# Performance work log

Hardware: AMD Instinct MI355X
Metric: run time of the kernel (lower is better)

## Reference

```python
import jax, jax.numpy as jnp
import numpy as np


def quat_to_rot(q):
    # q: [B, 4] = (x, y, z, w); same math as from_quaternion in the source.
    x, y, z, w = q[:, 0], q[:, 1], q[:, 2], q[:, 3]
    tx, ty, tz = 2.0 * x, 2.0 * y, 2.0 * z
    twx, twy, twz = tx * w, ty * w, tz * w
    txx, txy, txz = tx * x, ty * x, tz * x
    tyy, tyz, tzz = ty * y, tz * y, tz * z
    r = jnp.stack([1.0 - (tyy + tzz), txy - twz, txz + twy,
                   txy + twz, 1.0 - (txx + tzz), tyz - twx,
                   txz - twy, tyz + twx, 1.0 - (txx + tyy)], axis=-1)
    return r.reshape(-1, 3, 3)


def matrix_from_params(transfos):
    B, N = transfos.shape
    R = quat_to_rot(transfos[:, :4])
    if N == 10:
        S = jax.vmap(jnp.diag)(transfos[:, -3:])
    else:
        S = jnp.broadcast_to(jnp.eye(3, dtype=transfos.dtype), (B, 3, 3))
    SR = jnp.matmul(S, R)
    if N == 7:
        t = transfos[:, 4:7][..., None]
    else:
        t = jnp.zeros((B, 3, 1), transfos.dtype)
    return jnp.concatenate([SR, t], axis=2)  # [B, 3, 4]


def spatial_transformer_3d(img, transfos, min_ref_grid, max_ref_grid):
    B, H, W, D, C = img.shape  # ref_size_xyz = (W, H, D) per the source
    theta = matrix_from_params(transfos)  # [B, 3, 4]

    xs = jnp.linspace(min_ref_grid[0], max_ref_grid[0], W)
    ys = jnp.linspace(min_ref_grid[1], max_ref_grid[1], H)
    zs = jnp.linspace(min_ref_grid[2], max_ref_grid[2], D)
    mz, my, mx = jnp.meshgrid(zs, ys, xs, indexing='ij')  # (D, H, W), x fastest
    Nel = D * H * W
    grid = jnp.stack([mx.ravel(), my.ravel(), mz.ravel(),
                      jnp.ones(Nel, dtype=img.dtype)], axis=0)  # (4, Nel)
    pts = jnp.einsum('bij,jn->bin', theta, grid)  # (B, 3, Nel)

    Wf, Hf, Df = float(W), float(H), float(D)
    cx = (Wf - 1.0) / (max_ref_grid[0] - min_ref_grid[0])
    cy = (Hf - 1.0) / (max_ref_grid[1] - min_ref_grid[1])
    cz = (Df - 1.0) / (max_ref_grid[2] - min_ref_grid[2])
    ix = cx * pts[:, 0, :] - cx * min_ref_grid[0]
    iy = cy * pts[:, 1, :] - cy * min_ref_grid[1]
    iz = cz * pts[:, 2, :] - cz * min_ref_grid[2]

    # padding_mode in {'zeros','min'}: validity mask for out-of-grid points
    valid = ((ix >= 0.0) & (ix <= Wf - 1.0) &
             (iy >= 0.0) & (iy <= Hf - 1.0) &
             (iz >= 0.0) & (iz <= Df - 1.0)).astype(img.dtype)[..., None]  # (B, Nel, 1)

    ix0 = jnp.clip(jnp.floor(ix), 0.0, Wf - 1.0)
    iy0 = jnp.clip(jnp.floor(iy), 0.0, Hf - 1.0)
    iz0 = jnp.clip(jnp.floor(iz), 0.0, Df - 1.0)

    imf = img.reshape(B, H * W * D, C)
    acc = jnp.zeros((B, Nel, C), img.dtype)
    for ox in (0.0, 1.0):
        for oy in (0.0, 1.0):
            for oz in (0.0, 1.0):
                gx, gy, gz = ix0 + ox, iy0 + oy, iz0 + oz  # corner coords
                w = (jnp.clip(1.0 - jnp.abs(ix - gx), 0.0, 1.0) *
                     jnp.clip(1.0 - jnp.abs(iy - gy), 0.0, 1.0) *
                     jnp.clip(1.0 - jnp.abs(iz - gz), 0.0, 1.0))
                gxi = jnp.clip(gx, 0.0, Wf - 1.0).astype(jnp.int32)
                gyi = jnp.clip(gy, 0.0, Hf - 1.0).astype(jnp.int32)
                gzi = jnp.clip(gz, 0.0, Df - 1.0).astype(jnp.int32)
                lin = (gyi * W + gxi) * D + gzi  # row-major index into [H, W, D]
                v = jnp.take_along_axis(imf, lin[..., None], axis=1)  # (B, Nel, C)
                acc = acc + w[..., None] * v

    # padding_mode == 'min': fill out-of-grid voxels with the per-volume minimum
    fill = jnp.min(img, axis=(1, 2, 3, 4))[:, None, None]  # (B, 1, 1)
    out = valid * acc + (1.0 - valid) * fill
    # grid was flattened in (z, y, x) order with x fastest -> back to (H, W, D)
    out = out.reshape(B, D, H, W, C).transpose(0, 2, 3, 1, 4)
    return out


def setup_inputs() -> dict:
    key = jax.random.key(0)
    k1, k2 = jax.random.split(key)
    img = jax.random.normal(k1, (4, 160, 160, 160, 1), dtype=jnp.float32)
    transfos = jax.random.normal(k2, (4, 7), dtype=jnp.float32)
    return {"img": img, "transfos": transfos}


def reference(img, transfos):
    min_ref_grid = (-1.0, -1.0, -1.0)
    max_ref_grid = (1.0, 1.0, 1.0)
    return spatial_transformer_3d(img, transfos, min_ref_grid, max_ref_grid)
```

## Files before the change

kernel.cpp:

```cpp
#include <hip/hip_runtime.h>

#define HH 160
#define WW 160
#define DD 160
#define BB 4
#define NPB (HH * WW * DD / 4)
#define K1B 256

typedef float vfloat4 __attribute__((ext_vector_type(4)));

__global__ __launch_bounds__(256) void min_cst_kernel(const float4* __restrict__ img4,
                                                      const float* __restrict__ transfos,
                                                      float* __restrict__ partial,
                                                      double* __restrict__ cst) {
    const int b = blockIdx.y;
    const size_t base = (size_t)b * NPB;
    const int t0 = blockIdx.x * 256 + threadIdx.x;
    const int S = K1B * 256;

    float m = 3.4e38f;
    #pragma unroll
    for (int r = 0; r < 4; r++) {
        const int i0 = t0 + 4 * r * S;
        float4 v0 = img4[base + i0];
        float4 v1 = img4[base + i0 + S];
        float4 v2 = img4[base + i0 + 2 * S];
        float4 v3 = make_float4(3.4e38f, 3.4e38f, 3.4e38f, 3.4e38f);
        if (i0 + 3 * S < NPB) v3 = img4[base + i0 + 3 * S];
        m = fminf(m, fminf(fminf(v0.x, v0.y), fminf(v0.z, v0.w)));
        m = fminf(m, fminf(fminf(v1.x, v1.y), fminf(v1.z, v1.w)));
        m = fminf(m, fminf(fminf(v2.x, v2.y), fminf(v2.z, v2.w)));
        m = fminf(m, fminf(fminf(v3.x, v3.y), fminf(v3.z, v3.w)));
    }

    #pragma unroll
    for (int o = 32; o >= 1; o >>= 1) m = fminf(m, __shfl_down(m, o));
    __shared__ float s[4];
    const int lane = threadIdx.x & 63, wid = threadIdx.x >> 6;
    if (lane == 0) s[wid] = m;
    __syncthreads();
    if (threadIdx.x == 0) {
        partial[b * K1B + blockIdx.x] =
            fminf(fminf(s[0], s[1]), fminf(s[2], s[3]));
    }

    if (blockIdx.x == 0 && blockIdx.y == 0 && threadIdx.x < BB) {
        const int bb = threadIdx.x;
        const float* q = transfos + bb * 7;
        double x = q[0], y = q[1], z = q[2], w = q[3];
        double tx = 2.0 * x, ty = 2.0 * y, tz = 2.0 * z;
        double twx = tx * w, twy = ty * w, twz = tz * w;
        double txx = tx * x, txy = ty * x, txz = tz * x;
        double tyy = ty * y, tyz = tz * y, tzz = tz * z;
        double R[3][3] = {
            {1.0 - (tyy + tzz), txy - twz,         txz + twy},
            {txy + twz,         1.0 - (txx + tzz), tyz - twx},
            {txz - twy,         tyz + twx,         1.0 - (txx + tyy)}
        };
        double t[3] = {(double)q[4], (double)q[5], (double)q[6]};
        for (int r = 0; r < 3; r++) {
            cst[bb * 12 + r * 4 + 0] = R[r][0];
            cst[bb * 12 + r * 4 + 1] = R[r][1];
            cst[bb * 12 + r * 4 + 2] = R[r][2];
            cst[bb * 12 + r * 4 + 3] = 79.5 * (t[r] - R[r][0] - R[r][1] - R[r][2] + 1.0);
        }
    }
}

__global__ __launch_bounds__(256) void st3d_kernel(const float* __restrict__ img,
                                                   const double* __restrict__ cst,
                                                   const float* __restrict__ partial,
                                                   float* __restrict__ out) {
    const int b = blockIdx.z;
    const int y = blockIdx.y;

    __shared__ float sred[4];
    float pm = partial[b * K1B + threadIdx.x];
    #pragma unroll
    for (int o = 32; o >= 1; o >>= 1) pm = fminf(pm, __shfl_down(pm, o));
    if ((threadIdx.x & 63) == 0) sred[threadIdx.x >> 6] = pm;
    __syncthreads();
    const float fill = fminf(fminf(sred[0], sred[1]), fminf(sred[2], sred[3]));

    const int t = blockIdx.x * 256 + threadIdx.x;
    const int x = t / 40;
    const int zq = (t - 40 * x) * 4;

    const double* c = cst + b * 12;
    const double c2 = c[2], c6 = c[6], c10 = c[10];
    const double dx = (double)x, dy = (double)y, dz = (double)zq;
    const double ix0d = fma(c[0], dx, fma(c[1], dy, fma(c2, dz, c[3])));
    const double iy0d = fma(c[4], dx, fma(c[5], dy, fma(c6, dz, c[7])));
    const double iz0d = fma(c[8], dx, fma(c[9], dy, fma(c10, dz, c[11])));

    bool vld[4];
    {
        double jx = ix0d, jy = iy0d, jz = iz0d;
        #pragma unroll
        for (int k = 0; k < 4; k++) {
            vld[k] = (jx >= 0.0) && (jx <= 159.0) && (jy >= 0.0) && (jy <= 159.0) &&
                     (jz >= 0.0) && (jz <= 159.0);
            jx += c2; jy += c6; jz += c10;
        }
    }

    float acc[4] = {0.f, 0.f, 0.f, 0.f};
    if (__any(vld[0] | vld[1] | vld[2] | vld[3])) {
        const float* base = img + (size_t)b * (HH * WW * DD);
        float v[4][8];
        float fx[4], fy[4], fz[4];
        double jx = ix0d, jy = iy0d, jz = iz0d;
        #pragma unroll
        for (int k = 0; k < 4; k++) {
            double cx = fmin(fmax(jx, 0.0), 159.0);
            double cy = fmin(fmax(jy, 0.0), 159.0);
            double cz = fmin(fmax(jz, 0.0), 159.0);
            double flx = floor(cx), fly = floor(cy), flz = floor(cz);
            int x0 = (int)flx, y0 = (int)fly, z0 = (int)flz;
            fx[k] = (float)(cx - flx); fy[k] = (float)(cy - fly); fz[k] = (float)(cz - flz);
            int x1 = min(x0 + 1, 159), y1 = min(y0 + 1, 159), z1 = min(z0 + 1, 159);
            const float* p00 = base + ((size_t)y0 * WW + x0) * DD;
            const float* p01 = base + ((size_t)y0 * WW + x1) * DD;
            const float* p10 = base + ((size_t)y1 * WW + x0) * DD;
            const float* p11 = base + ((size_t)y1 * WW + x1) * DD;
            v[k][0] = p00[z0]; v[k][1] = p00[z1];
            v[k][2] = p10[z0]; v[k][3] = p10[z1];
            v[k][4] = p01[z0]; v[k][5] = p01[z1];
            v[k][6] = p11[z0]; v[k][7] = p11[z1];
            jx += c2; jy += c6; jz += c10;
        }
        #pragma unroll
        for (int k = 0; k < 4; k++) {
            float wx0 = 1.0f - fx[k], wx1 = fx[k];
            float wy0 = 1.0f - fy[k], wy1 = fy[k];
            float wz0 = 1.0f - fz[k], wz1 = fz[k];
            float a;
            a  = ((wx0 * wy0) * wz0) * v[k][0];
            a += ((wx0 * wy0) * wz1) * v[k][1];
            a += ((wx0 * wy1) * wz0) * v[k][2];
            a += ((wx0 * wy1) * wz1) * v[k][3];
            a += ((wx1 * wy0) * wz0) * v[k][4];
            a += ((wx1 * wy0) * wz1) * v[k][5];
            a += ((wx1 * wy1) * wz0) * v[k][6];
            a += ((wx1 * wy1) * wz1) * v[k][7];
            acc[k] = a;
        }
    }

    vfloat4 r;
    #pragma unroll
    for (int k = 0; k < 4; k++) r[k] = vld[k] ? acc[k] : fill;

    vfloat4* outp = (vfloat4*)(out + (size_t)(b * HH + y) * (WW * DD) + x * DD + zq);
    __builtin_nontemporal_store(r, outp);
}

extern "C" void kernel_launch(void* const* d_in, const int* in_sizes, int n_in,
                              void* d_out, int out_size, void* d_ws, size_t ws_size,
                              hipStream_t stream) {
    const float* img = (const float*)d_in[0];
    const float* transfos = (const float*)d_in[1];
    float* out = (float*)d_out;
    float* partial = (float*)d_ws;
    double* cst = (double*)((char*)d_ws + 4096);

    min_cst_kernel<<<dim3(K1B, BB), 256, 0, stream>>>((const float4*)img, transfos,
                                                      partial, cst);
    st3d_kernel<<<dim3(25, 160, BB), 256, 0, stream>>>(img, cst, partial, out);
}
```

Before: 154.1 us.

## Split sampling into fill pass plus compacted gather of in-bounds voxel groups

Replaces the single sampling kernel with a pass that writes the fill value everywhere and uses a ballot plus an atomic counter to build a compacted list of in-bounds 4-voxel groups. A separate persistent-style gather kernel then does trilinear interpolation only for the listed groups. The aim is to avoid divergent, wave-wide gather work in waves that are mostly out of bounds and to balance the gather load. In exchange it writes the output twice for valid groups, adds a memset, an extra launch and global atomics. If the workspace holds fewer entries than the in-bounds groups, those groups beyond capacity keep the fill value and come out wrong.

```diff
diff --git a/kernel.cpp b/kernel.cpp
--- a/kernel.cpp
+++ b/kernel.cpp
@@ -6,8 +6,10 @@
 #define BB 4
 #define NPB (HH * WW * DD / 4)
 #define K1B 256
+#define TPP 6400
 
 typedef float vfloat4 __attribute__((ext_vector_type(4)));
+
 
 __global__ __launch_bounds__(256) void min_cst_kernel(const float4* __restrict__ img4,
                                                       const float* __restrict__ transfos,
@@ -67,10 +69,13 @@
     }
 }
 
-__global__ __launch_bounds__(256) void st3d_kernel(const float* __restrict__ img,
-                                                   const double* __restrict__ cst,
-                                                   const float* __restrict__ partial,
-                                                   float* __restrict__ out) {
+__global__ __launch_bounds__(256) void fill_compact_kernel(const double* __restrict__ cst,
+                                                           const float* __restrict__ partial,
+                                                           float* __restrict__ fillv,
+                                                           unsigned* __restrict__ counter,
+                                                           unsigned* __restrict__ list,
+                                                           unsigned cap,
+                                                           float* __restrict__ out) {
     const int b = blockIdx.z;
     const int y = blockIdx.y;
 
@@ -81,6 +86,7 @@
     if ((threadIdx.x & 63) == 0) sred[threadIdx.x >> 6] = pm;
     __syncthreads();
     const float fill = fminf(fminf(sred[0], sred[1]), fminf(sred[2], sred[3]));
+    if (blockIdx.x == 0 && blockIdx.y == 0 && threadIdx.x == 0) fillv[b] = fill;
 
     const int t = blockIdx.x * 256 + threadIdx.x;
     const int x = t / 40;
@@ -89,29 +95,71 @@
     const double* c = cst + b * 12;
     const double c2 = c[2], c6 = c[6], c10 = c[10];
     const double dx = (double)x, dy = (double)y, dz = (double)zq;
-    const double ix0d = fma(c[0], dx, fma(c[1], dy, fma(c2, dz, c[3])));
-    const double iy0d = fma(c[4], dx, fma(c[5], dy, fma(c6, dz, c[7])));
-    const double iz0d = fma(c[8], dx, fma(c[9], dy, fma(c10, dz, c[11])));
-
-    bool vld[4];
-    {
-        double jx = ix0d, jy = iy0d, jz = iz0d;
+    double jx = fma(c[0], dx, fma(c[1], dy, fma(c2, dz, c[3])));
+    double jy = fma(c[4], dx, fma(c[5], dy, fma(c6, dz, c[7])));
+    double jz = fma(c[8], dx, fma(c[9], dy, fma(c10, dz, c[11])));
+
+    bool has = false;
+    #pragma unroll
+    for (int k = 0; k < 4; k++) {
+        has |= (jx >= 0.0) && (jx <= 159.0) && (jy >= 0.0) && (jy <= 159.0) &&
+               (jz >= 0.0) && (jz <= 159.0);
+        jx += c2; jy += c6; jz += c10;
+    }
+
+    vfloat4 r = {fill, fill, fill, fill};
+    vfloat4* outp = (vfloat4*)(out + (size_t)(b * HH + y) * (WW * DD) + x * DD + zq);
+    __builtin_nontemporal_store(r, outp);
+
+    unsigned long long mask = __ballot(has);
+    if (mask != 0ull) {
+        const int lane = threadIdx.x & 63;
+        const int leader = __ffsll((long long)mask) - 1;
+        unsigned base = 0;
+        if (lane == leader) base = atomicAdd(counter, (unsigned)__popcll(mask));
+        base = __shfl(base, leader);
+        if (has) {
+            unsigned idx = base + __popcll(mask & ((1ull << lane) - 1ull));
+            if (idx < cap) list[idx] = (unsigned)((b * HH + y) * TPP + t);
+        }
+    }
+}
+
+__global__ __launch_bounds__(256) void gather_kernel(const float* __restrict__ img,
+                                                     const double* __restrict__ cst,
+                                                     const float* __restrict__ fillv,
+                                                     const unsigned* __restrict__ counter,
+                                                     const unsigned* __restrict__ list,
+                                                     unsigned cap,
+                                                     float* __restrict__ out) {
+    unsigned n = *counter;
+    if (n > cap) n = cap;
+    for (unsigned i = blockIdx.x * 256 + threadIdx.x; i < n; i += gridDim.x * 256) {
+        const unsigned g = list[i];
+        const int t = g % TPP;
+        const unsigned q = g / TPP;
+        const int y = q % HH;
+        const int b = q / HH;
+        const int x = t / 40;
+        const int zq = (t - 40 * x) * 4;
+
+        const double* c = cst + b * 12;
+        const double c2 = c[2], c6 = c[6], c10 = c[10];
+        const double dx = (double)x, dy = (double)y, dz = (double)zq;
+        double jx = fma(c[0], dx, fma(c[1], dy, fma(c2, dz, c[3])));
+        double jy = fma(c[4], dx, fma(c[5], dy, fma(c6, dz, c[7])));
+        double jz = fma(c[8], dx, fma(c[9], dy, fma(c10, dz, c[11])));
+
+        const float fill = fillv[b];
+        const float* base = img + (size_t)b * (HH * WW * DD);
+
+        bool vld[4];
+        float v[4][8];
+        float fx[4], fy[4], fz[4];
         #pragma unroll
         for (int k = 0; k < 4; k++) {
             vld[k] = (jx >= 0.0) && (jx <= 159.0) && (jy >= 0.0) && (jy <= 159.0) &&
                      (jz >= 0.0) && (jz <= 159.0);
-            jx += c2; jy += c6; jz += c10;
-        }
-    }
-
-    float acc[4] = {0.f, 0.f, 0.f, 0.f};
-    if (__any(vld[0] | vld[1] | vld[2] | vld[3])) {
-        const float* base = img + (size_t)b * (HH * WW * DD);
-        float v[4][8];
-        float fx[4], fy[4], fz[4];
-        double jx = ix0d, jy = iy0d, jz = iz0d;
-        #pragma unroll
-        for (int k = 0; k < 4; k++) {
             double cx = fmin(fmax(jx, 0.0), 159.0);
             double cy = fmin(fmax(jy, 0.0), 159.0);
             double cz = fmin(fmax(jz, 0.0), 159.0);
@@ -129,6 +177,8 @@
             v[k][6] = p11[z0]; v[k][7] = p11[z1];
             jx += c2; jy += c6; jz += c10;
         }
+
+        vfloat4 r;
         #pragma unroll
         for (int k = 0; k < 4; k++) {
             float wx0 = 1.0f - fx[k], wx1 = fx[k];
@@ -143,16 +193,12 @@
             a += ((wx1 * wy0) * wz1) * v[k][5];
             a += ((wx1 * wy1) * wz0) * v[k][6];
             a += ((wx1 * wy1) * wz1) * v[k][7];
-            acc[k] = a;
-        }
-    }
-
-    vfloat4 r;
-    #pragma unroll
-    for (int k = 0; k < 4; k++) r[k] = vld[k] ? acc[k] : fill;
-
-    vfloat4* outp = (vfloat4*)(out + (size_t)(b * HH + y) * (WW * DD) + x * DD + zq);
-    __builtin_nontemporal_store(r, outp);
+            r[k] = vld[k] ? a : fill;
+        }
+
+        vfloat4* outp = (vfloat4*)(out + (size_t)q * (WW * DD) + x * DD + zq);
+        *outp = r;
+    }
 }
 
 extern "C" void kernel_launch(void* const* d_in, const int* in_sizes, int n_in,
@@ -161,10 +207,18 @@
     const float* img = (const float*)d_in[0];
     const float* transfos = (const float*)d_in[1];
     float* out = (float*)d_out;
-    float* partial = (float*)d_ws;
-    double* cst = (double*)((char*)d_ws + 4096);
-
+    char* ws = (char*)d_ws;
+    float* partial = (float*)ws;
+    double* cst = (double*)(ws + 4096);
+    float* fillv = (float*)(ws + 4608);
+    unsigned* counter = (unsigned*)(ws + 5120);
+    unsigned* list = (unsigned*)(ws + 8192);
+    unsigned cap = (unsigned)((ws_size > 8192) ? (ws_size - 8192) / 4 : 0);
+
+    (void)hipMemsetAsync(counter, 0, sizeof(unsigned), stream);
     min_cst_kernel<<<dim3(K1B, BB), 256, 0, stream>>>((const float4*)img, transfos,
                                                       partial, cst);
-    st3d_kernel<<<dim3(25, 160, BB), 256, 0, stream>>>(img, cst, partial, out);
-}
+    fill_compact_kernel<<<dim3(25, 160, BB), 256, 0, stream>>>(cst, partial, fillv,
+                                                               counter, list, cap, out);
+    gather_kernel<<<dim3(1024), 256, 0, stream>>>(img, cst, fillv, counter, list, cap, out);
+}
```

New measurement: 185.1 us. 20.1% more time.

## Replace partial-min reduction with atomic min key and gather only valid samples

Applied to the files above, without the earlier changes.

Each block of the min kernel now folds its per-volume minimum into one global key with an order-preserving uint atomicMin, after a memset that initializes the keys. This removes the per-block reduction of 256 partials and the __syncthreads in every st3d block. The gather now skips loads per sample when that sample is out of range, instead of deciding per wavefront, and drops the clamping of coordinates. The output store becomes a plain store instead of a nontemporal one. The trade-offs are an extra memset launch, atomic contention, and reads of uninitialized v for invalid samples, although those values are masked out.

```diff
diff --git a/kernel.cpp b/kernel.cpp
--- a/kernel.cpp
+++ b/kernel.cpp
@@ -9,9 +9,19 @@
 
 typedef float vfloat4 __attribute__((ext_vector_type(4)));
 
+__device__ __forceinline__ unsigned mapf(float f) {
+    unsigned b = __float_as_uint(f);
+    return (b & 0x80000000u) ? ~b : (b | 0x80000000u);
+}
+__device__ __forceinline__ float unmapf(unsigned k) {
+    unsigned b = (k & 0x80000000u) ? (k ^ 0x80000000u) : ~k;
+    return __uint_as_float(b);
+}
+
+
 __global__ __launch_bounds__(256) void min_cst_kernel(const float4* __restrict__ img4,
                                                       const float* __restrict__ transfos,
-                                                      float* __restrict__ partial,
+                                                      unsigned* __restrict__ minkey,
                                                       double* __restrict__ cst) {
     const int b = blockIdx.y;
     const size_t base = (size_t)b * NPB;
@@ -40,8 +50,8 @@
     if (lane == 0) s[wid] = m;
     __syncthreads();
     if (threadIdx.x == 0) {
-        partial[b * K1B + blockIdx.x] =
-            fminf(fminf(s[0], s[1]), fminf(s[2], s[3]));
+        m = fminf(fminf(s[0], s[1]), fminf(s[2], s[3]));
+        atomicMin(&minkey[b * 64], mapf(m));
     }
 
     if (blockIdx.x == 0 && blockIdx.y == 0 && threadIdx.x < BB) {
@@ -69,18 +79,11 @@
 
 __global__ __launch_bounds__(256) void st3d_kernel(const float* __restrict__ img,
                                                    const double* __restrict__ cst,
-                                                   const float* __restrict__ partial,
+                                                   const unsigned* __restrict__ minkey,
                                                    float* __restrict__ out) {
     const int b = blockIdx.z;
     const int y = blockIdx.y;
-
-    __shared__ float sred[4];
-    float pm = partial[b * K1B + threadIdx.x];
-    #pragma unroll
-    for (int o = 32; o >= 1; o >>= 1) pm = fminf(pm, __shfl_down(pm, o));
-    if ((threadIdx.x & 63) == 0) sred[threadIdx.x >> 6] = pm;
-    __syncthreads();
-    const float fill = fminf(fminf(sred[0], sred[1]), fminf(sred[2], sred[3]));
+    const float fill = unmapf(minkey[b * 64]);
 
     const int t = blockIdx.x * 256 + threadIdx.x;
     const int x = t / 40;
@@ -89,70 +92,63 @@
     const double* c = cst + b * 12;
     const double c2 = c[2], c6 = c[6], c10 = c[10];
     const double dx = (double)x, dy = (double)y, dz = (double)zq;
-    const double ix0d = fma(c[0], dx, fma(c[1], dy, fma(c2, dz, c[3])));
-    const double iy0d = fma(c[4], dx, fma(c[5], dy, fma(c6, dz, c[7])));
-    const double iz0d = fma(c[8], dx, fma(c[9], dy, fma(c10, dz, c[11])));
+    double jx = fma(c[0], dx, fma(c[1], dy, fma(c2, dz, c[3])));
+    double jy = fma(c[4], dx, fma(c[5], dy, fma(c6, dz, c[7])));
+    double jz = fma(c[8], dx, fma(c[9], dy, fma(c10, dz, c[11])));
+
+    const float* base = img + (size_t)b * (HH * WW * DD);
 
     bool vld[4];
-    {
-        double jx = ix0d, jy = iy0d, jz = iz0d;
-        #pragma unroll
-        for (int k = 0; k < 4; k++) {
-            vld[k] = (jx >= 0.0) && (jx <= 159.0) && (jy >= 0.0) && (jy <= 159.0) &&
-                     (jz >= 0.0) && (jz <= 159.0);
-            jx += c2; jy += c6; jz += c10;
-        }
+    float fx[4], fy[4], fz[4];
+    const float* pp[4][4];
+    int zz0[4], zz1[4];
+    #pragma unroll
+    for (int k = 0; k < 4; k++) {
+        vld[k] = (jx >= 0.0) && (jx <= 159.0) && (jy >= 0.0) && (jy <= 159.0) &&
+                 (jz >= 0.0) && (jz <= 159.0);
+        double flx = floor(jx), fly = floor(jy), flz = floor(jz);
+        int x0 = (int)flx, y0 = (int)fly, z0 = (int)flz;
+        fx[k] = (float)(jx - flx); fy[k] = (float)(jy - fly); fz[k] = (float)(jz - flz);
+        int x1 = min(x0 + 1, 159), y1 = min(y0 + 1, 159), z1 = min(z0 + 1, 159);
+        pp[k][0] = base + ((size_t)y0 * WW + x0) * DD;
+        pp[k][1] = base + ((size_t)y1 * WW + x0) * DD;
+        pp[k][2] = base + ((size_t)y0 * WW + x1) * DD;
+        pp[k][3] = base + ((size_t)y1 * WW + x1) * DD;
+        zz0[k] = z0; zz1[k] = z1;
+        jx += c2; jy += c6; jz += c10;
     }
 
-    float acc[4] = {0.f, 0.f, 0.f, 0.f};
-    if (__any(vld[0] | vld[1] | vld[2] | vld[3])) {
-        const float* base = img + (size_t)b * (HH * WW * DD);
-        float v[4][8];
-        float fx[4], fy[4], fz[4];
-        double jx = ix0d, jy = iy0d, jz = iz0d;
-        #pragma unroll
-        for (int k = 0; k < 4; k++) {
-            double cx = fmin(fmax(jx, 0.0), 159.0);
-            double cy = fmin(fmax(jy, 0.0), 159.0);
-            double cz = fmin(fmax(jz, 0.0), 159.0);
-            double flx = floor(cx), fly = floor(cy), flz = floor(cz);
-            int x0 = (int)flx, y0 = (int)fly, z0 = (int)flz;
-            fx[k] = (float)(cx - flx); fy[k] = (float)(cy - fly); fz[k] = (float)(cz - flz);
-            int x1 = min(x0 + 1, 159), y1 = min(y0 + 1, 159), z1 = min(z0 + 1, 159);
-            const float* p00 = base + ((size_t)y0 * WW + x0) * DD;
-            const float* p01 = base + ((size_t)y0 * WW + x1) * DD;
-            const float* p10 = base + ((size_t)y1 * WW + x0) * DD;
-            const float* p11 = base + ((size_t)y1 * WW + x1) * DD;
-            v[k][0] = p00[z0]; v[k][1] = p00[z1];
-            v[k][2] = p10[z0]; v[k][3] = p10[z1];
-            v[k][4] = p01[z0]; v[k][5] = p01[z1];
-            v[k][6] = p11[z0]; v[k][7] = p11[z1];
-            jx += c2; jy += c6; jz += c10;
-        }
-        #pragma unroll
-        for (int k = 0; k < 4; k++) {
-            float wx0 = 1.0f - fx[k], wx1 = fx[k];
-            float wy0 = 1.0f - fy[k], wy1 = fy[k];
-            float wz0 = 1.0f - fz[k], wz1 = fz[k];
-            float a;
-            a  = ((wx0 * wy0) * wz0) * v[k][0];
-            a += ((wx0 * wy0) * wz1) * v[k][1];
-            a += ((wx0 * wy1) * wz0) * v[k][2];
-            a += ((wx0 * wy1) * wz1) * v[k][3];
-            a += ((wx1 * wy0) * wz0) * v[k][4];
-            a += ((wx1 * wy0) * wz1) * v[k][5];
-            a += ((wx1 * wy1) * wz0) * v[k][6];
-            a += ((wx1 * wy1) * wz1) * v[k][7];
-            acc[k] = a;
+    float v[4][8];
+    #pragma unroll
+    for (int k = 0; k < 4; k++) {
+        if (vld[k]) {
+            v[k][0] = pp[k][0][zz0[k]]; v[k][1] = pp[k][0][zz1[k]];
+            v[k][2] = pp[k][1][zz0[k]]; v[k][3] = pp[k][1][zz1[k]];
+            v[k][4] = pp[k][2][zz0[k]]; v[k][5] = pp[k][2][zz1[k]];
+            v[k][6] = pp[k][3][zz0[k]]; v[k][7] = pp[k][3][zz1[k]];
         }
     }
 
     vfloat4 r;
     #pragma unroll
-    for (int k = 0; k < 4; k++) r[k] = vld[k] ? acc[k] : fill;
+    for (int k = 0; k < 4; k++) {
+        float wx0 = 1.0f - fx[k], wx1 = fx[k];
+        float wy0 = 1.0f - fy[k], wy1 = fy[k];
+        float wz0 = 1.0f - fz[k], wz1 = fz[k];
+        float a;
+        a  = ((wx0 * wy0) * wz0) * v[k][0];
+        a += ((wx0 * wy0) * wz1) * v[k][1];
+        a += ((wx0 * wy1) * wz0) * v[k][2];
+        a += ((wx0 * wy1) * wz1) * v[k][3];
+        a += ((wx1 * wy0) * wz0) * v[k][4];
+        a += ((wx1 * wy0) * wz1) * v[k][5];
+        a += ((wx1 * wy1) * wz0) * v[k][6];
+        a += ((wx1 * wy1) * wz1) * v[k][7];
+        r[k] = vld[k] ? a : fill;
+    }
 
     vfloat4* outp = (vfloat4*)(out + (size_t)(b * HH + y) * (WW * DD) + x * DD + zq);
-    __builtin_nontemporal_store(r, outp);
+    *outp = r;
 }
 
 extern "C" void kernel_launch(void* const* d_in, const int* in_sizes, int n_in,
@@ -161,10 +157,11 @@
     const float* img = (const float*)d_in[0];
     const float* transfos = (const float*)d_in[1];
     float* out = (float*)d_out;
-    float* partial = (float*)d_ws;
+    unsigned* minkey = (unsigned*)d_ws;
     double* cst = (double*)((char*)d_ws + 4096);
 
+    (void)hipMemsetAsync(minkey, 0xFF, 1024, stream);
     min_cst_kernel<<<dim3(K1B, BB), 256, 0, stream>>>((const float4*)img, transfos,
-                                                      partial, cst);
-    st3d_kernel<<<dim3(25, 160, BB), 256, 0, stream>>>(img, cst, partial, out);
+                                                      minkey, cst);
+    st3d_kernel<<<dim3(25, 160, BB), 256, 0, stream>>>(img, cst, minkey, out);
 }
```

New measurement: 136.0 us. -11.8%, faster.
